# Kernel optimization log

Measured on AMD Instinct MI355X. Metric: run time of the kernel, lower is better.

## Reference

```python
import jax, jax.numpy as jnp
import numpy as np

IN_F = 4096
OUT_F = 4096
BATCH = 8192


def setup_inputs() -> dict:
    key = jax.random.key(0)
    ks = jax.random.split(key, 7)
    bound = 1.0 / np.sqrt(IN_F)
    return {
        "x": jax.random.normal(ks[0], (BATCH, IN_F), dtype=jnp.float32),
        "weight_mu": jax.random.normal(ks[1], (OUT_F, IN_F), dtype=jnp.float32) * np.sqrt(2.0 / IN_F),  # kaiming fan_in relu
        "weight_log_var": jnp.full((OUT_F, IN_F), -6.0, dtype=jnp.float32),
        "bias_mu": jax.random.uniform(ks[2], (OUT_F,), dtype=jnp.float32, minval=-bound, maxval=bound),
        "bias_log_var": jnp.full((OUT_F,), -6.0, dtype=jnp.float32),
        "weight_eps": jax.random.normal(ks[3], (OUT_F, IN_F), dtype=jnp.float32),
        "bias_eps": jax.random.normal(ks[4], (OUT_F,), dtype=jnp.float32),
    }


def reference(x, weight_mu, weight_log_var, bias_mu, bias_log_var, weight_eps, bias_eps):
    # Reparameterized sampling: w = mu + eps * exp(0.5 * log_var)
    weight = weight_mu + weight_eps * jnp.exp(0.5 * weight_log_var)   # [out, in]
    bias = bias_mu + bias_eps * jnp.exp(0.5 * bias_log_var)           # [out]
    # F.linear(x, weight, bias) = x @ weight.T + bias
    return jnp.einsum("bi,oi->bo", x, weight) + bias
```

## Files before the change

### kernel.cpp

```cpp
#include <hip/hip_runtime.h>
#include <hip/hip_bf16.h>
#include <stdint.h>

typedef __bf16 bf16x8 __attribute__((ext_vector_type(8)));
typedef float f32x4 __attribute__((ext_vector_type(4)));
typedef unsigned short u16x8 __attribute__((ext_vector_type(8)));

__device__ inline unsigned short f2bf_rne(float f) {
  unsigned int u = __float_as_uint(f);
  u += 0x7fffu + ((u >> 16) & 1u);
  return (unsigned short)(u >> 16);
}

__global__ __launch_bounds__(256) void prep_weight(
    const float4* __restrict__ mu, const float4* __restrict__ lv,
    const float4* __restrict__ eps, u16x8* __restrict__ wbf, int n8) {
  int i = blockIdx.x * 256 + threadIdx.x;
  if (i >= n8) return;
  float4 m0 = mu[2 * i], m1 = mu[2 * i + 1];
  float4 v0 = lv[2 * i], v1 = lv[2 * i + 1];
  float4 e0 = eps[2 * i], e1 = eps[2 * i + 1];
  u16x8 p;
  p[0] = f2bf_rne(m0.x + e0.x * __expf(0.5f * v0.x));
  p[1] = f2bf_rne(m0.y + e0.y * __expf(0.5f * v0.y));
  p[2] = f2bf_rne(m0.z + e0.z * __expf(0.5f * v0.z));
  p[3] = f2bf_rne(m0.w + e0.w * __expf(0.5f * v0.w));
  p[4] = f2bf_rne(m1.x + e1.x * __expf(0.5f * v1.x));
  p[5] = f2bf_rne(m1.y + e1.y * __expf(0.5f * v1.y));
  p[6] = f2bf_rne(m1.z + e1.z * __expf(0.5f * v1.z));
  p[7] = f2bf_rne(m1.w + e1.w * __expf(0.5f * v1.w));
  wbf[i] = p;
}

__global__ __launch_bounds__(256) void prep_x(
    const float4* __restrict__ x, u16x8* __restrict__ xbf, int n8) {
  int i = blockIdx.x * 256 + threadIdx.x;
  if (i >= n8) return;
  float4 m0 = x[2 * i], m1 = x[2 * i + 1];
  u16x8 p;
  p[0] = f2bf_rne(m0.x); p[1] = f2bf_rne(m0.y);
  p[2] = f2bf_rne(m0.z); p[3] = f2bf_rne(m0.w);
  p[4] = f2bf_rne(m1.x); p[5] = f2bf_rne(m1.y);
  p[6] = f2bf_rne(m1.z); p[7] = f2bf_rne(m1.w);
  xbf[i] = p;
}

__global__ __launch_bounds__(512, 2) void gemm_bt_bias(
    const unsigned short* __restrict__ A,
    const unsigned short* __restrict__ B,
    const float* __restrict__ bmu, const float* __restrict__ blv,
    const float* __restrict__ beps,
    float* __restrict__ C, int M, int N, int K) {
  __shared__ __align__(16) unsigned short As[2][2][128 * 64];
  __shared__ __align__(16) unsigned short Bs[2][2][128 * 64];

  const int tid  = threadIdx.x;
  const int wave = tid >> 6;
  const int lane = tid & 63;
  const int wm = wave >> 2;
  const int wn = wave & 3;

  const int rowA0 = blockIdx.y * 256;
  const int rowB0 = blockIdx.x * 256;

  const int srow = tid >> 3;
  const int scol = ((tid & 7) ^ (srow & 7)) * 8;
  const unsigned short* pA = A + (size_t)(rowA0 + srow) * K + scol;
  const unsigned short* pB = B + (size_t)(rowB0 + srow) * K + scol;
  const int dep = wave * 512;

#define GLL(srcp, dstp)                                                     \
  __builtin_amdgcn_global_load_lds(                                         \
      (const __attribute__((address_space(1))) unsigned int*)(srcp),        \
      (__attribute__((address_space(3))) unsigned int*)(dstp), 16, 0, 0)

#define STAGE_A(kt, b, h) do {                                              \
    const unsigned short* s_ = pA + (size_t)((h) * 128) * K + (size_t)(kt) * 64; \
    GLL(s_, &As[b][h][dep]);                                                \
    GLL(s_ + (size_t)64 * K, &As[b][h][4096 + dep]); } while (0)
#define STAGE_B(kt, b, h) do {                                              \
    const unsigned short* s_ = pB + (size_t)((h) * 128) * K + (size_t)(kt) * 64; \
    GLL(s_, &Bs[b][h][dep]);                                                \
    GLL(s_ + (size_t)64 * K, &Bs[b][h][4096 + dep]); } while (0)

  f32x4 acc[8][4];
#pragma unroll
  for (int i = 0; i < 8; ++i)
#pragma unroll
    for (int j = 0; j < 4; ++j)
      acc[i][j] = (f32x4){0.f, 0.f, 0.f, 0.f};

  const int mrow = lane & 15;
  const int gsel = lane >> 4;
  const int pgL = (gsel ^ (mrow & 7)) * 8;
  const int pgH = ((4 + gsel) ^ (mrow & 7)) * 8;
  const int aoff = mrow * 64;
  const int boff = ((wn & 1) * 64 + mrow) * 64;

  STAGE_A(0, 0, 0); STAGE_A(0, 0, 1); STAGE_B(0, 0, 0); STAGE_B(0, 0, 1);
  STAGE_A(1, 1, 0); STAGE_A(1, 1, 1); STAGE_B(1, 1, 0); STAGE_B(1, 1, 1);
  asm volatile("s_waitcnt vmcnt(8)" ::: "memory");
  __builtin_amdgcn_s_barrier();
  __builtin_amdgcn_sched_barrier(0);

  bf16x8 a0[4][2], a1[4][2], b01[2][2], b23[2][2];

  const int NT = K / 64;
  for (int t = 0; t < NT; ++t) {
    const int c = t & 1;
    const unsigned short* as_ = &As[c][wm][0];
    const unsigned short* bs_ = &Bs[c][wn >> 1][0];
    const bool pf = (t + 2 < NT);
    const bool pr = (t + 1 < NT);

#pragma unroll
    for (int mi = 0; mi < 4; ++mi) {
      a0[mi][0] = *(const bf16x8*)&as_[aoff + mi * 1024 + pgL];
      a0[mi][1] = *(const bf16x8*)&as_[aoff + mi * 1024 + pgH];
    }
#pragma unroll
    for (int ni = 0; ni < 2; ++ni) {
      b01[ni][0] = *(const bf16x8*)&bs_[boff + ni * 1024 + pgL];
      b01[ni][1] = *(const bf16x8*)&bs_[boff + ni * 1024 + pgH];
    }
#pragma unroll
    for (int mi = 0; mi < 4; ++mi) {
      a1[mi][0] = *(const bf16x8*)&as_[aoff + (mi + 4) * 1024 + pgL];
      a1[mi][1] = *(const bf16x8*)&as_[aoff + (mi + 4) * 1024 + pgH];
    }

    __builtin_amdgcn_s_setprio(1);
#pragma unroll
    for (int kk = 0; kk < 2; ++kk)
#pragma unroll
      for (int mi = 0; mi < 4; ++mi)
#pragma unroll
        for (int ni = 0; ni < 2; ++ni)
          acc[mi][ni] = __builtin_amdgcn_mfma_f32_16x16x32_bf16(
              a0[mi][kk], b01[ni][kk], acc[mi][ni], 0, 0, 0);
    __builtin_amdgcn_s_setprio(0);

#pragma unroll
    for (int ni = 0; ni < 2; ++ni) {
      b23[ni][0] = *(const bf16x8*)&bs_[boff + (ni + 2) * 1024 + pgL];
      b23[ni][1] = *(const bf16x8*)&bs_[boff + (ni + 2) * 1024 + pgH];
    }

    __builtin_amdgcn_s_setprio(1);
#pragma unroll
    for (int kk = 0; kk < 2; ++kk)
#pragma unroll
      for (int mi = 0; mi < 4; ++mi)
#pragma unroll
        for (int ni = 0; ni < 2; ++ni)
          acc[mi + 4][ni] = __builtin_amdgcn_mfma_f32_16x16x32_bf16(
              a1[mi][kk], b01[ni][kk], acc[mi + 4][ni], 0, 0, 0);
    __builtin_amdgcn_s_setprio(0);

    asm volatile("s_waitcnt lgkmcnt(0)" ::: "memory");
    __builtin_amdgcn_sched_barrier(0);
    __builtin_amdgcn_s_barrier();
    __builtin_amdgcn_sched_barrier(0);

    if (pf) {
      STAGE_A(t + 2, c, 0); STAGE_A(t + 2, c, 1);
      STAGE_B(t + 2, c, 0); STAGE_B(t + 2, c, 1);
    }

    __builtin_amdgcn_s_setprio(1);
#pragma unroll
    for (int kk = 0; kk < 2; ++kk)
#pragma unroll
      for (int mi = 0; mi < 4; ++mi)
#pragma unroll
        for (int ni = 0; ni < 2; ++ni)
          acc[mi + 4][ni + 2] = __builtin_amdgcn_mfma_f32_16x16x32_bf16(
              a1[mi][kk], b23[ni][kk], acc[mi + 4][ni + 2], 0, 0, 0);
    __builtin_amdgcn_s_setprio(0);

    __builtin_amdgcn_s_setprio(1);
#pragma unroll
    for (int kk = 0; kk < 2; ++kk)
#pragma unroll
      for (int mi = 0; mi < 4; ++mi)
#pragma unroll
        for (int ni = 0; ni < 2; ++ni)
          acc[mi][ni + 2] = __builtin_amdgcn_mfma_f32_16x16x32_bf16(
              a0[mi][kk], b23[ni][kk], acc[mi][ni + 2], 0, 0, 0);
    __builtin_amdgcn_s_setprio(0);

    if (pr) {
      if (pf) { asm volatile("s_waitcnt vmcnt(8)" ::: "memory"); }
      else    { asm volatile("s_waitcnt vmcnt(0)" ::: "memory"); }
      __builtin_amdgcn_sched_barrier(0);
      __builtin_amdgcn_s_barrier();
      __builtin_amdgcn_sched_barrier(0);
    }
  }

  const int colq = lane & 15;
  const int rq4  = (lane >> 4) * 4;
#pragma unroll
  for (int ni = 0; ni < 4; ++ni) {
    const int col = rowB0 + wn * 64 + ni * 16 + colq;
    const float bias = bmu[col] + beps[col] * __expf(0.5f * blv[col]);
#pragma unroll
    for (int mi = 0; mi < 8; ++mi) {
      const int rbase = rowA0 + wm * 128 + mi * 16 + rq4;
#pragma unroll
      for (int r = 0; r < 4; ++r)
        C[(size_t)(rbase + r) * N + col] = acc[mi][ni][r] + bias;
    }
  }
#undef GLL
#undef STAGE_A
#undef STAGE_B
}

extern "C" void kernel_launch(void* const* d_in, const int* in_sizes, int n_in,
                              void* d_out, int out_size, void* d_ws, size_t ws_size,
                              hipStream_t stream) {
  const float* x    = (const float*)d_in[0];
  const float* wmu  = (const float*)d_in[1];
  const float* wlv  = (const float*)d_in[2];
  const float* bmu  = (const float*)d_in[3];
  const float* blv  = (const float*)d_in[4];
  const float* weps = (const float*)d_in[5];
  const float* beps = (const float*)d_in[6];
  float* out = (float*)d_out;

  const int M = 8192, N = 4096, K = 4096;

  unsigned short* xbf = (unsigned short*)d_ws;
  unsigned short* wbf = xbf + (size_t)M * K;

  const int n8w = N * K / 8;
  prep_weight<<<n8w / 256, 256, 0, stream>>>(
      (const float4*)wmu, (const float4*)wlv, (const float4*)weps,
      (u16x8*)wbf, n8w);
  const int n8x = M * K / 8;
  prep_x<<<n8x / 256, 256, 0, stream>>>((const float4*)x, (u16x8*)xbf, n8x);

  dim3 grid(N / 256, M / 256);
  gemm_bt_bias<<<grid, 512, 0, stream>>>(xbf, wbf, bmu, blv, beps, out, M, N, K);
}
```

Measured before the change: 603.6 us.

## Split GEMM main loop into barrier-separated phases interleaving prefetch with MFMA

Restructures each K iteration into four compute phases separated by workgroup barriers. The next tile's global-to-LDS loads are spread across those phases: A low rows, then A high rows, then B. This lets waves overlap LDS reads and memory traffic with MFMA work instead of issuing all prefetches at one point. In exchange it adds several more barriers per iteration. Some prefetch loads may also be issued before other waves' LDS reads have finished, which risks a race.

Measured after the change: 620.2 us. 2.7% more time.

```diff
diff --git a/kernel.cpp b/kernel.cpp
--- a/kernel.cpp
+++ b/kernel.cpp
@@ -74,14 +74,19 @@
       (const __attribute__((address_space(1))) unsigned int*)(srcp),        \
       (__attribute__((address_space(3))) unsigned int*)(dstp), 16, 0, 0)
 
-#define STAGE_A(kt, b, h) do {                                              \
-    const unsigned short* s_ = pA + (size_t)((h) * 128) * K + (size_t)(kt) * 64; \
-    GLL(s_, &As[b][h][dep]);                                                \
-    GLL(s_ + (size_t)64 * K, &As[b][h][4096 + dep]); } while (0)
-#define STAGE_B(kt, b, h) do {                                              \
-    const unsigned short* s_ = pB + (size_t)((h) * 128) * K + (size_t)(kt) * 64; \
-    GLL(s_, &Bs[b][h][dep]);                                                \
-    GLL(s_ + (size_t)64 * K, &Bs[b][h][4096 + dep]); } while (0)
+#define SA_LO(kt, b, h) GLL(pA + (size_t)((h) * 128) * K + (size_t)(kt) * 64, \
+                            &As[b][h][dep])
+#define SA_HI(kt, b, h) GLL(pA + (size_t)((h) * 128 + 64) * K + (size_t)(kt) * 64, \
+                            &As[b][h][4096 + dep])
+#define SB_LO(kt, b, h) GLL(pB + (size_t)((h) * 128) * K + (size_t)(kt) * 64, \
+                            &Bs[b][h][dep])
+#define SB_HI(kt, b, h) GLL(pB + (size_t)((h) * 128 + 64) * K + (size_t)(kt) * 64, \
+                            &Bs[b][h][4096 + dep])
+
+#define FENCE() __builtin_amdgcn_sched_barrier(0)
+#define BAR1()  do { FENCE(); __builtin_amdgcn_s_barrier(); FENCE(); } while (0)
+#define DRAIN() do { asm volatile("s_waitcnt lgkmcnt(0)" ::: "memory"); FENCE(); } while (0)
+#define BAR2()  do { FENCE(); __builtin_amdgcn_s_barrier(); FENCE(); } while (0)
 
   f32x4 acc[8][4];
 #pragma unroll
@@ -97,11 +102,13 @@
   const int aoff = mrow * 64;
   const int boff = ((wn & 1) * 64 + mrow) * 64;
 
-  STAGE_A(0, 0, 0); STAGE_A(0, 0, 1); STAGE_B(0, 0, 0); STAGE_B(0, 0, 1);
-  STAGE_A(1, 1, 0); STAGE_A(1, 1, 1); STAGE_B(1, 1, 0); STAGE_B(1, 1, 1);
+  SA_LO(0, 0, 0); SA_LO(0, 0, 1); SA_HI(0, 0, 0); SA_HI(0, 0, 1);
+  SB_LO(0, 0, 0); SB_LO(0, 0, 1); SB_HI(0, 0, 0); SB_HI(0, 0, 1);
+  SA_LO(1, 1, 0); SA_LO(1, 1, 1); SA_HI(1, 1, 0); SA_HI(1, 1, 1);
+  SB_LO(1, 1, 0); SB_LO(1, 1, 1); SB_HI(1, 1, 0); SB_HI(1, 1, 1);
   asm volatile("s_waitcnt vmcnt(8)" ::: "memory");
   __builtin_amdgcn_s_barrier();
-  __builtin_amdgcn_sched_barrier(0);
+  FENCE();
 
   bf16x8 a0[4][2], a1[4][2], b01[2][2], b23[2][2];
 
@@ -123,50 +130,45 @@
       b01[ni][0] = *(const bf16x8*)&bs_[boff + ni * 1024 + pgL];
       b01[ni][1] = *(const bf16x8*)&bs_[boff + ni * 1024 + pgH];
     }
+    BAR1(); DRAIN();
+    __builtin_amdgcn_s_setprio(1);
+#pragma unroll
+    for (int kk = 0; kk < 2; ++kk)
+#pragma unroll
+      for (int mi = 0; mi < 4; ++mi)
+#pragma unroll
+        for (int ni = 0; ni < 2; ++ni)
+          acc[mi][ni] = __builtin_amdgcn_mfma_f32_16x16x32_bf16(
+              a0[mi][kk], b01[ni][kk], acc[mi][ni], 0, 0, 0);
+    __builtin_amdgcn_s_setprio(0);
+    BAR2();
+
 #pragma unroll
     for (int mi = 0; mi < 4; ++mi) {
       a1[mi][0] = *(const bf16x8*)&as_[aoff + (mi + 4) * 1024 + pgL];
       a1[mi][1] = *(const bf16x8*)&as_[aoff + (mi + 4) * 1024 + pgH];
     }
-
-    __builtin_amdgcn_s_setprio(1);
-#pragma unroll
-    for (int kk = 0; kk < 2; ++kk)
-#pragma unroll
-      for (int mi = 0; mi < 4; ++mi)
-#pragma unroll
-        for (int ni = 0; ni < 2; ++ni)
-          acc[mi][ni] = __builtin_amdgcn_mfma_f32_16x16x32_bf16(
-              a0[mi][kk], b01[ni][kk], acc[mi][ni], 0, 0, 0);
-    __builtin_amdgcn_s_setprio(0);
+    if (pf) { SA_LO(t + 2, c, 0); SA_LO(t + 2, c, 1); }
+    BAR1(); DRAIN();
+    __builtin_amdgcn_s_setprio(1);
+#pragma unroll
+    for (int kk = 0; kk < 2; ++kk)
+#pragma unroll
+      for (int mi = 0; mi < 4; ++mi)
+#pragma unroll
+        for (int ni = 0; ni < 2; ++ni)
+          acc[mi + 4][ni] = __builtin_amdgcn_mfma_f32_16x16x32_bf16(
+              a1[mi][kk], b01[ni][kk], acc[mi + 4][ni], 0, 0, 0);
+    __builtin_amdgcn_s_setprio(0);
+    BAR2();
 
 #pragma unroll
     for (int ni = 0; ni < 2; ++ni) {
       b23[ni][0] = *(const bf16x8*)&bs_[boff + (ni + 2) * 1024 + pgL];
       b23[ni][1] = *(const bf16x8*)&bs_[boff + (ni + 2) * 1024 + pgH];
     }
-
-    __builtin_amdgcn_s_setprio(1);
-#pragma unroll
-    for (int kk = 0; kk < 2; ++kk)
-#pragma unroll
-      for (int mi = 0; mi < 4; ++mi)
-#pragma unroll
-        for (int ni = 0; ni < 2; ++ni)
-          acc[mi + 4][ni] = __builtin_amdgcn_mfma_f32_16x16x32_bf16(
-              a1[mi][kk], b01[ni][kk], acc[mi + 4][ni], 0, 0, 0);
-    __builtin_amdgcn_s_setprio(0);
-
-    asm volatile("s_waitcnt lgkmcnt(0)" ::: "memory");
-    __builtin_amdgcn_sched_barrier(0);
-    __builtin_amdgcn_s_barrier();
-    __builtin_amdgcn_sched_barrier(0);
-
-    if (pf) {
-      STAGE_A(t + 2, c, 0); STAGE_A(t + 2, c, 1);
-      STAGE_B(t + 2, c, 0); STAGE_B(t + 2, c, 1);
-    }
-
+    if (pf) { SA_HI(t + 2, c, 0); SA_HI(t + 2, c, 1); }
+    BAR1(); DRAIN();
     __builtin_amdgcn_s_setprio(1);
 #pragma unroll
     for (int kk = 0; kk < 2; ++kk)
@@ -177,7 +179,13 @@
           acc[mi + 4][ni + 2] = __builtin_amdgcn_mfma_f32_16x16x32_bf16(
               a1[mi][kk], b23[ni][kk], acc[mi + 4][ni + 2], 0, 0, 0);
     __builtin_amdgcn_s_setprio(0);
-
+    BAR2();
+
+    if (pf) {
+      SB_LO(t + 2, c, 0); SB_LO(t + 2, c, 1);
+      SB_HI(t + 2, c, 0); SB_HI(t + 2, c, 1);
+    }
+    BAR1();
     __builtin_amdgcn_s_setprio(1);
 #pragma unroll
     for (int kk = 0; kk < 2; ++kk)
@@ -188,14 +196,12 @@
           acc[mi][ni + 2] = __builtin_amdgcn_mfma_f32_16x16x32_bf16(
               a0[mi][kk], b23[ni][kk], acc[mi][ni + 2], 0, 0, 0);
     __builtin_amdgcn_s_setprio(0);
-
     if (pr) {
       if (pf) { asm volatile("s_waitcnt vmcnt(8)" ::: "memory"); }
       else    { asm volatile("s_waitcnt vmcnt(0)" ::: "memory"); }
-      __builtin_amdgcn_sched_barrier(0);
-      __builtin_amdgcn_s_barrier();
-      __builtin_amdgcn_sched_barrier(0);
-    }
+      FENCE();
+    }
+    BAR2();
   }
 
   const int colq = lane & 15;
@@ -213,8 +219,14 @@
     }
   }
 #undef GLL
-#undef STAGE_A
-#undef STAGE_B
+#undef SA_LO
+#undef SA_HI
+#undef SB_LO
+#undef SB_HI
+#undef FENCE
+#undef BAR1
+#undef DRAIN
+#undef BAR2
 }
 
 extern "C" void kernel_launch(void* const* d_in, const int* in_sizes, int n_in,
```
